# Performance work log

Measured on AMD Instinct MI355X. Metric: run time of the kernel, lower is better.

Reference implementation:

```python
import jax, jax.numpy as jnp
import numpy as np

D = 768      # d_model (BERT-base)
H = 8        # MatTransformer heads
DK = D // H  # 96
L = 4        # MatTransformer layers
FF = 1024    # MatTransformer hidden_size
NREL = 97    # num_relations
BAG = 8      # bag_len (docs per bag)
SEQ = 512    # seq_len
NB = 3       # bridge entities per doc
S = 2 + NB   # spans per doc: h, t, bridges
E = BAG * S  # total entities = 40
NEG = -1e30


def setup_inputs() -> dict:
    key = jax.random.key(0)
    ks = jax.random.split(key, 30)
    w = lambda k, shp: jax.random.normal(k, shp, jnp.float32) * 0.02
    inp = {
        "embedding": jax.random.normal(ks[0], (BAG, SEQ, D), jnp.float32),
        "spans": jnp.sort(jax.random.randint(ks[1], (BAG, S, 2), 0, SEQ, jnp.int32), axis=-1),
        # Codred pairwise-relation params (torch Linear stored as [in, out])
        "wu_w": w(ks[2], (D, D)), "wu_b": jnp.zeros((D,), jnp.float32),
        "wvv_w": w(ks[3], (D, D)), "wvv_b": jnp.zeros((D,), jnp.float32),
        "lnr_w": w(ks[4], (D, D)), "lnr_b": jnp.zeros((D,), jnp.float32),
        # MatTransformer params, stacked over layers
        "matt_wq": w(ks[5], (L, D, D)), "matt_bq": jnp.zeros((L, D), jnp.float32),
        "matt_wk": w(ks[6], (L, D, D)), "matt_bk": jnp.zeros((L, D), jnp.float32),
        "matt_wv": w(ks[7], (L, D, D)), "matt_bv": jnp.zeros((L, D), jnp.float32),
        "matt_wo": w(ks[8], (L, D, D)), "matt_bo": jnp.zeros((L, D), jnp.float32),
        "matt_w1": w(ks[9], (L, D, FF)), "matt_b1": jnp.zeros((L, FF), jnp.float32),
        "matt_w2": w(ks[10], (L, FF, D)), "matt_b2": jnp.zeros((L, D), jnp.float32),
        "matt_g1": jnp.ones((L, D), jnp.float32), "matt_be1": jnp.zeros((L, D), jnp.float32),
        "matt_g2": jnp.ones((L, D), jnp.float32), "matt_be2": jnp.zeros((L, D), jnp.float32),
        # relation predictor
        "pred_w": w(ks[11], (D, NREL)), "pred_b": jnp.zeros((NREL,), jnp.float32),
    }
    return inp


def _layernorm(x, g, b, eps=1e-5):
    m = jnp.mean(x, axis=-1, keepdims=True)
    v = jnp.var(x, axis=-1, keepdims=True)
    return (x - m) * jax.lax.rsqrt(v + eps) * g + b


def reference(embedding, spans, wu_w, wu_b, wvv_w, wvv_b, lnr_w, lnr_b,
              matt_wq, matt_bq, matt_wk, matt_bk, matt_wv, matt_bv, matt_wo, matt_bo,
              matt_w1, matt_b1, matt_w2, matt_b2, matt_g1, matt_be1, matt_g2, matt_be2,
              pred_w, pred_b):
    # --- entity span max-pool (gather + max over inclusive [start, end]) ---
    pos = jnp.arange(SEQ)
    span_mask = (pos[None, None, :] >= spans[..., 0:1]) & (pos[None, None, :] <= spans[..., 1:2])  # [BAG,S,SEQ]
    pooled = jnp.max(jnp.where(span_mask[..., None], embedding[:, None, :, :], NEG), axis=2)  # [BAG,S,D]
    htb = pooled.reshape(E, D)  # per-doc order: h, t, b1..bNB (matches htb_embs stacking)

    # --- pairwise relation matrix: relu(ln1(relu(u_i + v_j))) ---
    u = htb @ wu_w + wu_b                       # [E,D]
    v = htb @ wvv_w + wvv_b                     # [E,D]
    alpha = jax.nn.relu(u[:, None, :] + v[None, :, :])          # [E,E,D]
    rel = jax.nn.relu(alpha @ lnr_w + lnr_b)                    # [E,E,D]

    # --- MatTransformer: encoder over the E*E relation tokens (rel_mask all ones) ---
    T = E * E
    x = rel.reshape(T, D)
    scale = 1.0 / np.sqrt(DK).astype(np.float32)
    for l in range(L):
        q = (x @ matt_wq[l] + matt_bq[l]).reshape(T, H, DK)
        k = (x @ matt_wk[l] + matt_bk[l]).reshape(T, H, DK)
        vv = (x @ matt_wv[l] + matt_bv[l]).reshape(T, H, DK)
        scores = jnp.einsum('thd,shd->hts', q, k) * scale       # [H,T,T]
        attn = jax.nn.softmax(scores, axis=-1)
        o = jnp.einsum('hts,shd->thd', attn, vv).reshape(T, D)
        o = o @ matt_wo[l] + matt_bo[l]
        x = _layernorm(x + o, matt_g1[l], matt_be1[l])
        ff = jax.nn.relu(x @ matt_w1[l] + matt_b1[l]) @ matt_w2[l] + matt_b2[l]
        x = _layernorm(x + ff, matt_g2[l], matt_be2[l])
    rel_m = x.reshape(E, E, D)

    # --- gather (h, t) relation features, predict, bag max-pool over logits ---
    h_pos = jnp.arange(BAG) * S      # head entity index per doc
    t_pos = h_pos + 1                # tail entity index per doc
    ht_feat = rel_m[h_pos, t_pos]    # [BAG,D]
    ht_logits = ht_feat @ pred_w + pred_b          # [BAG,NREL]
    bag_logit = jnp.max(ht_logits, axis=0, keepdims=True)  # [1,NREL]
    return bag_logit
```

## Files before the change

### kernel.cpp

```cpp
#include <hip/hip_runtime.h>


#define D    768
#define H    8
#define DKD  96
#define LAY  4
#define FFD  1024
#define NREL 97
#define BAG  8
#define SPANS 5
#define E    40
#define TT   1600
#define SEQ  512
#define D3   2304
#define NS   3

typedef __attribute__((ext_vector_type(8))) short bf16x8;
typedef __attribute__((ext_vector_type(4))) float f32x4;
typedef unsigned short ushort_t;
typedef unsigned int uint_t;

__device__ __forceinline__ ushort_t f2b(float x) {
    uint_t u = __builtin_bit_cast(uint_t, x);
    return (ushort_t)((u + 0x7fffu + ((u >> 16) & 1u)) >> 16);
}
__device__ __forceinline__ float b2f(ushort_t v) {
    return __builtin_bit_cast(float, (uint_t)v << 16);
}

__device__ __forceinline__ void gload16(const void* g, void* l) {
    __builtin_amdgcn_global_load_lds(
        (const __attribute__((address_space(1))) unsigned int*)g,
        (__attribute__((address_space(3))) unsigned int*)l, 16, 0, 0);
}

__device__ __forceinline__ float block_sum(float v, float* red) {
#pragma unroll
    for (int o = 32; o >= 1; o >>= 1) v += __shfl_xor(v, o);
    __syncthreads();
    if ((threadIdx.x & 63) == 0) red[threadIdx.x >> 6] = v;
    __syncthreads();
    return red[0] + red[1] + red[2] + red[3];
}

__global__ __launch_bounds__(256) void span_pool_p1(const float* __restrict__ emb,
        const int* __restrict__ spans, float* __restrict__ partial) {
    const int e = blockIdx.x, pg = blockIdx.y;
    const int bag = e / SPANS;
    const int st = spans[e * 2 + 0];
    const int en = spans[e * 2 + 1];
    const int p0 = max(st, pg * 64);
    const int p1 = min(en, pg * 64 + 63);
    const int tid = threadIdx.x;
    if (tid >= 192) return;
    float4 m = make_float4(-1e30f, -1e30f, -1e30f, -1e30f);
    for (int p = p0; p <= p1; ++p) {
        const float4 v = *(const float4*)(emb + ((size_t)bag * SEQ + p) * D + tid * 4);
        m.x = fmaxf(m.x, v.x); m.y = fmaxf(m.y, v.y);
        m.z = fmaxf(m.z, v.z); m.w = fmaxf(m.w, v.w);
    }
    *(float4*)(partial + ((size_t)e * 8 + pg) * D + tid * 4) = m;
}

__global__ __launch_bounds__(256) void span_pool_p2(const float* __restrict__ partial,
        ushort_t* __restrict__ htb) {
    const int e = blockIdx.x;
    const int tid = threadIdx.x;
    if (tid >= 192) return;
    float4 m = make_float4(-1e30f, -1e30f, -1e30f, -1e30f);
#pragma unroll
    for (int pg = 0; pg < 8; ++pg) {
        const float4 v = *(const float4*)(partial + ((size_t)e * 8 + pg) * D + tid * 4);
        m.x = fmaxf(m.x, v.x); m.y = fmaxf(m.y, v.y);
        m.z = fmaxf(m.z, v.z); m.w = fmaxf(m.w, v.w);
    }
    ushort4 o;
    o.x = f2b(m.x); o.y = f2b(m.y); o.z = f2b(m.z); o.w = f2b(m.w);
    *(ushort4*)(htb + (size_t)e * D + tid * 4) = o;
}

__global__ __launch_bounds__(256) void alpha_k(const float* __restrict__ uv,
        ushort_t* __restrict__ a) {
    const int ij = blockIdx.x;
    const int i = ij / E, j = ij % E;
    const int tid = threadIdx.x;
#pragma unroll
    for (int t2 = 0; t2 < 3; ++t2) {
        const int d = tid + t2 * 256;
        a[(size_t)ij * D + d] =
            f2b(fmaxf(uv[(size_t)i * 1536 + d] + uv[(size_t)j * 1536 + 768 + d], 0.f));
    }
}

__global__ __launch_bounds__(256) void transpose_up(const float* __restrict__ lnr,
        const float* __restrict__ wu, const float* __restrict__ wvv,
        ushort_t* __restrict__ lnrT, ushort_t* __restrict__ wuvT) {
    __shared__ float t[32][33];
    const int z = blockIdx.z;
    const float* src = (z == 0) ? lnr : (z == 1) ? wu : wvv;
    ushort_t* dst = (z == 0) ? lnrT : wuvT + (size_t)(z - 1) * D * D;
    const int n0 = blockIdx.x * 32, k0 = blockIdx.y * 32;
    const int tx = threadIdx.x & 31, ty = threadIdx.x >> 5;
#pragma unroll
    for (int i = 0; i < 4; ++i)
        t[ty + i * 8][tx] = src[(size_t)(k0 + ty + i * 8) * D + n0 + tx];
    __syncthreads();
#pragma unroll
    for (int i = 0; i < 4; ++i)
        dst[(size_t)(n0 + ty + i * 8) * D + k0 + tx] = f2b(t[tx][ty + i * 8]);
}

__global__ __launch_bounds__(256) void transpose_layer(const float* __restrict__ wq,
        const float* __restrict__ wk, const float* __restrict__ wv,
        const float* __restrict__ wo, const float* __restrict__ w1,
        const float* __restrict__ w2, int l, ushort_t* __restrict__ wT4,
        ushort_t* __restrict__ w1T, ushort_t* __restrict__ w2T) {
    __shared__ float t[32][33];
    const int z = blockIdx.z;
    const float* src; ushort_t* dst; int K, N;
    if (z < 4) {
        K = D; N = D;
        src = (z == 0 ? wq : z == 1 ? wk : z == 2 ? wv : wo) + (size_t)l * D * D;
        dst = wT4 + (size_t)z * D * D;
    } else if (z == 4) {
        K = D; N = FFD; src = w1 + (size_t)l * D * FFD; dst = w1T;
    } else {
        K = FFD; N = D; src = w2 + (size_t)l * FFD * D; dst = w2T;
    }
    const int n0 = blockIdx.x * 32, k0 = blockIdx.y * 32;
    if (n0 >= N || k0 >= K) return;
    const int tx = threadIdx.x & 31, ty = threadIdx.x >> 5;
#pragma unroll
    for (int i = 0; i < 4; ++i)
        t[ty + i * 8][tx] = src[(size_t)(k0 + ty + i * 8) * N + n0 + tx];
    __syncthreads();
#pragma unroll
    for (int i = 0; i < 4; ++i)
        dst[(size_t)(n0 + ty + i * 8) * K + k0 + tx] = f2b(t[tx][ty + i * 8]);
}

__global__ __launch_bounds__(256) void concat_bias(const float* __restrict__ bq,
        const float* __restrict__ bk, const float* __restrict__ bv,
        const float* __restrict__ bu, const float* __restrict__ bvv,
        float* __restrict__ bqkv, float* __restrict__ buv) {
    const int i = blockIdx.x * 256 + threadIdx.x;
    if (i < LAY * D3) {
        const int l = i / D3, j = i % D3;
        bqkv[i] = j < D ? bq[l * D + j] : j < 2 * D ? bk[l * D + j - D] : bv[l * D + j - 2 * D];
    }
    const int k = i - LAY * D3;
    if (k >= 0 && k < 2 * D) buv[k] = k < D ? bu[k] : bvv[k - D];
}

template<int RELU, int SCALEQ>
__global__ __launch_bounds__(256) void gemm_mfma(const ushort_t* __restrict__ A,
        const ushort_t* __restrict__ Bt, const float* __restrict__ bias,
        float* __restrict__ Cf, ushort_t* __restrict__ Cb, int M, int N, int K) {
    __shared__ ushort_t As[2][128 * 32];
    __shared__ ushort_t Bs[2][64 * 32];
    const int tid = threadIdx.x;
    const int lane = tid & 63, w = tid >> 6;
    const int l15 = lane & 15, lg = lane >> 4;
    const int bm = blockIdx.y * 128, bn = blockIdx.x * 64;
    const int wm = (w >> 1) * 64, wn = (w & 1) * 32;
    const int trA0 = w * 32 + (lane >> 2);
    const int trA1 = trA0 + 16;
    const int trB  = w * 16 + (lane >> 2);
    const int sc   = (lane & 3) * 8;
    const size_t rowA0 = (size_t)min(bm + trA0, M - 1) * K;
    const size_t rowA1 = (size_t)min(bm + trA1, M - 1) * K;
    const size_t rowB  = (size_t)(bn + trB) * K;

    f32x4 acc[4][2];
#pragma unroll
    for (int mi = 0; mi < 4; ++mi)
#pragma unroll
        for (int ni = 0; ni < 2; ++ni)
            acc[mi][ni] = (f32x4){0.f, 0.f, 0.f, 0.f};

    auto STAGE = [&](int buf, int k0) {
        gload16(A + rowA0 + k0 + sc, As[buf] + w * 1024);
        gload16(A + rowA1 + k0 + sc, As[buf] + w * 1024 + 512);
        gload16(Bt + rowB + k0 + sc, Bs[buf] + w * 512);
    };

    const int ntk = K / 32;
    STAGE(0, 0);
    __syncthreads();
    for (int t = 0; t < ntk; ++t) {
        const int buf = t & 1;
        if (t + 1 < ntk) STAGE(buf ^ 1, (t + 1) * 32);
        bf16x8 af[4], bfr[2];
#pragma unroll
        for (int mi = 0; mi < 4; ++mi)
            af[mi] = *(const bf16x8*)&As[buf][(wm + mi * 16 + l15) * 32 + lg * 8];
#pragma unroll
        for (int ni = 0; ni < 2; ++ni)
            bfr[ni] = *(const bf16x8*)&Bs[buf][(wn + ni * 16 + l15) * 32 + lg * 8];
        __builtin_amdgcn_s_setprio(1);
#pragma unroll
        for (int mi = 0; mi < 4; ++mi)
#pragma unroll
            for (int ni = 0; ni < 2; ++ni)
                acc[mi][ni] = __builtin_amdgcn_mfma_f32_16x16x32_bf16(
                    af[mi], bfr[ni], acc[mi][ni], 0, 0, 0);
        __builtin_amdgcn_s_setprio(0);
        __syncthreads();
    }
#pragma unroll
    for (int mi = 0; mi < 4; ++mi)
#pragma unroll
        for (int ni = 0; ni < 2; ++ni)
#pragma unroll
            for (int r = 0; r < 4; ++r) {
                const int row = bm + wm + mi * 16 + lg * 4 + r;
                if (row >= M) continue;
                const int col = bn + wn + ni * 16 + l15;
                float v = acc[mi][ni][r] + bias[col];
                if (RELU) v = fmaxf(v, 0.f);
                if (SCALEQ) { if (col < D) v *= 0.10206207261596577f; }
                if (Cf) Cf[(size_t)row * N + col] = v;
                if (Cb) Cb[(size_t)row * N + col] = f2b(v);
            }
}

__global__ __launch_bounds__(256) void attn_part(const ushort_t* __restrict__ qkv,
        ushort_t* __restrict__ Opart, float* __restrict__ ml) {
    __shared__ ushort_t Ks[64][104];
    __shared__ ushort_t Vt[96][72];
    __shared__ ushort_t Ps[4][16][72];
    const int q0 = blockIdx.x * 64;
    const int h = blockIdx.y;
    const int cch = blockIdx.z;
    const int t_lo = (cch * (TT / 64)) / NS;
    const int t_hi = ((cch + 1) * (TT / 64)) / NS;
    const int tid = threadIdx.x;
    const int lane = tid & 63, w = tid >> 6;
    const int l15 = lane & 15, lg = lane >> 4;

    int r_[3], c_[3];
#pragma unroll
    for (int i = 0; i < 3; ++i) {
        const int ch = i * 256 + tid;
        r_[i] = ch / 12; c_[i] = (ch % 12) * 8;
    }
    bf16x8 qfrag[3];
#pragma unroll
    for (int ks = 0; ks < 3; ++ks)
        qfrag[ks] = *(const bf16x8*)(qkv + (size_t)(q0 + w * 16 + l15) * D3
                                     + h * DKD + ks * 32 + lg * 8);
    uint4 kreg[3], vreg[3];
    {
        const int s0 = t_lo * 64;
#pragma unroll
        for (int i = 0; i < 3; ++i) {
            kreg[i] = *(const uint4*)(qkv + (size_t)(s0 + r_[i]) * D3 + D + h * DKD + c_[i]);
            vreg[i] = *(const uint4*)(qkv + (size_t)(s0 + r_[i]) * D3 + 2 * D + h * DKD + c_[i]);
        }
    }
    float m_run[4], l_run[4];
    f32x4 acc_o[6];
#pragma unroll
    for (int r = 0; r < 4; ++r) { m_run[r] = -1e30f; l_run[r] = 0.f; }
#pragma unroll
    for (int nt = 0; nt < 6; ++nt) acc_o[nt] = (f32x4){0.f, 0.f, 0.f, 0.f};

    for (int t = t_lo; t < t_hi; ++t) {
        __syncthreads();
#pragma unroll
        for (int i = 0; i < 3; ++i) {
            *(uint4*)&Ks[r_[i]][c_[i]] = kreg[i];
            const ushort_t* pv = (const ushort_t*)&vreg[i];
            const int kk = r_[i] ^ (((c_[i] >> 3) & 7) << 3);
#pragma unroll
            for (int j = 0; j < 8; ++j) Vt[c_[i] + j][kk] = pv[j];
        }
        __syncthreads();
        if (t + 1 < t_hi) {
            const int s0 = (t + 1) * 64;
#pragma unroll
            for (int i = 0; i < 3; ++i) {
                kreg[i] = *(const uint4*)(qkv + (size_t)(s0 + r_[i]) * D3 + D + h * DKD + c_[i]);
                vreg[i] = *(const uint4*)(qkv + (size_t)(s0 + r_[i]) * D3 + 2 * D + h * DKD + c_[i]);
            }
        }
        f32x4 accs[4];
#pragma unroll
        for (int ni = 0; ni < 4; ++ni) accs[ni] = (f32x4){0.f, 0.f, 0.f, 0.f};
        __builtin_amdgcn_s_setprio(1);
#pragma unroll
        for (int ks = 0; ks < 3; ++ks) {
#pragma unroll
            for (int ni = 0; ni < 4; ++ni) {
                const bf16x8 bk = *(const bf16x8*)&Ks[ni * 16 + l15][ks * 32 + lg * 8];
                accs[ni] = __builtin_amdgcn_mfma_f32_16x16x32_bf16(qfrag[ks], bk, accs[ni], 0, 0, 0);
            }
        }
        __builtin_amdgcn_s_setprio(0);
        float mx[4];
#pragma unroll
        for (int r = 0; r < 4; ++r) {
            mx[r] = fmaxf(fmaxf(accs[0][r], accs[1][r]), fmaxf(accs[2][r], accs[3][r]));
#pragma unroll
            for (int o = 1; o <= 8; o <<= 1) mx[r] = fmaxf(mx[r], __shfl_xor(mx[r], o));
        }
        const bool grow = (mx[0] > m_run[0] + 8.f) || (mx[1] > m_run[1] + 8.f) ||
                          (mx[2] > m_run[2] + 8.f) || (mx[3] > m_run[3] + 8.f);
        if (__any(grow)) {
#pragma unroll
            for (int r = 0; r < 4; ++r) {
                const float mnew = fmaxf(m_run[r], mx[r]);
                const float sf = __expf(m_run[r] - mnew);
                m_run[r] = mnew;
                l_run[r] *= sf;
#pragma unroll
                for (int nt = 0; nt < 6; ++nt) acc_o[nt][r] *= sf;
            }
        }
        float ps[4][4];
#pragma unroll
        for (int r = 0; r < 4; ++r) {
            float rs = 0.f;
#pragma unroll
            for (int ni = 0; ni < 4; ++ni) {
                ps[ni][r] = __expf(accs[ni][r] - m_run[r]);
                rs += ps[ni][r];
            }
#pragma unroll
            for (int o = 1; o <= 8; o <<= 1) rs += __shfl_xor(rs, o);
            l_run[r] += rs;
        }
#pragma unroll
        for (int ni = 0; ni < 4; ++ni)
#pragma unroll
            for (int r = 0; r < 4; ++r)
                Ps[w][lg * 4 + r][ni * 16 + l15] = f2b(ps[ni][r]);
        __builtin_amdgcn_s_setprio(1);
#pragma unroll
        for (int ks = 0; ks < 2; ++ks) {
            const bf16x8 ap = *(const bf16x8*)&Ps[w][l15][ks * 32 + lg * 8];
#pragma unroll
            for (int nt = 0; nt < 6; ++nt) {
                const int dim = nt * 16 + l15;
                const int kcol = (ks * 32 + lg * 8) ^ (((dim >> 3) & 7) << 3);
                const bf16x8 bv = *(const bf16x8*)&Vt[dim][kcol];
                acc_o[nt] = __builtin_amdgcn_mfma_f32_16x16x32_bf16(ap, bv, acc_o[nt], 0, 0, 0);
            }
        }
        __builtin_amdgcn_s_setprio(0);
    }
    __syncthreads();
    ushort_t* scr = &Ks[0][0] + w * (16 * 104);
#pragma unroll
    for (int nt = 0; nt < 6; ++nt)
#pragma unroll
        for (int r = 0; r < 4; ++r)
            scr[(lg * 4 + r) * 104 + nt * 16 + l15] = f2b(acc_o[nt][r]);
    const size_t obase = (((size_t)cch * H + h) * TT + q0 + w * 16) * DKD;
#pragma unroll
    for (int ch = 0; ch < 3; ++ch) {
        const int idx = ch * 64 + lane;
        const int row = idx / 12;
        const int c16 = (idx % 12) * 8;
        const uint4 v = *(const uint4*)&scr[row * 104 + c16];
        *(uint4*)(Opart + obase + (size_t)row * DKD + c16) = v;
    }
    if (l15 == 0) {
#pragma unroll
        for (int r = 0; r < 4; ++r) {
            const int row = q0 + w * 16 + lg * 4 + r;
            float2* mlp = (float2*)ml;
            mlp[((size_t)cch * H + h) * TT + row] = make_float2(m_run[r], l_run[r]);
        }
    }
}

__global__ __launch_bounds__(256) void attn_combine(const ushort_t* __restrict__ Opart,
        const float* __restrict__ ml, ushort_t* __restrict__ O) {
    const int row = blockIdx.x;
    const int tid = threadIdx.x;
    const float2* mlp = (const float2*)ml;
#pragma unroll
    for (int kk = 0; kk < 3; ++kk) {
        const int col = tid + kk * 256;
        const int h = col / DKD, d = col % DKD;
        float m[NS], l[NS], M = -1e30f;
#pragma unroll
        for (int c = 0; c < NS; ++c) {
            const float2 v = mlp[((size_t)c * H + h) * TT + row];
            m[c] = v.x; l[c] = v.y; M = fmaxf(M, m[c]);
        }
        float L = 0.f, o = 0.f;
#pragma unroll
        for (int c = 0; c < NS; ++c) {
            const float e = __expf(m[c] - M);
            L += l[c] * e;
            o += b2f(Opart[(((size_t)c * H + h) * TT + row) * DKD + d]) * e;
        }
        O[(size_t)row * D + col] = f2b(o / L);
    }
}

__global__ __launch_bounds__(256) void add_ln(float* __restrict__ x,
        const float* __restrict__ y, const float* __restrict__ g,
        const float* __restrict__ b, ushort_t* __restrict__ xb) {
    __shared__ float red[4];
    const int row = blockIdx.x;
    const int tid = threadIdx.x;
    float vals[3];
    float s = 0.f;
#pragma unroll
    for (int i = 0; i < 3; ++i) {
        const int c = tid + i * 256;
        const float t = x[(size_t)row * D + c] + y[(size_t)row * D + c];
        vals[i] = t; s += t;
    }
    const float mean = block_sum(s, red) * (1.f / 768.f);
    float s2 = 0.f;
#pragma unroll
    for (int i = 0; i < 3; ++i) { const float dd = vals[i] - mean; s2 += dd * dd; }
    const float var = block_sum(s2, red) * (1.f / 768.f);
    const float inv = rsqrtf(var + 1e-5f);
#pragma unroll
    for (int i = 0; i < 3; ++i) {
        const int c = tid + i * 256;
        const float o = (vals[i] - mean) * inv * g[c] + b[c];
        x[(size_t)row * D + c] = o;
        xb[(size_t)row * D + c] = f2b(o);
    }
}

__global__ __launch_bounds__(256) void predict_k(const float* __restrict__ x,
        const float* __restrict__ pw, const float* __restrict__ pb,
        float* __restrict__ out) {
    __shared__ float red[4];
    const int r = blockIdx.x;
    const int tid = threadIdx.x;
    float best = -1e30f;
    for (int bag = 0; bag < BAG; ++bag) {
        const int row = (bag * SPANS) * E + (bag * SPANS + 1);
        const float* f = x + (size_t)row * D;
        float acc = 0.f;
        for (int d = tid; d < D; d += 256) acc += f[d] * pw[(size_t)d * NREL + r];
        best = fmaxf(best, block_sum(acc, red));
    }
    if (tid == 0) out[r] = best + pb[r];
}

extern "C" void kernel_launch(void* const* d_in, const int* in_sizes, int n_in,
                              void* d_out, int out_size, void* d_ws, size_t ws_size,
                              hipStream_t stream) {
    const float* emb  = (const float*)d_in[0];
    const int*  spans = (const int*)d_in[1];
    const float* wu_w = (const float*)d_in[2];  const float* wu_b = (const float*)d_in[3];
    const float* wvv_w= (const float*)d_in[4];  const float* wvv_b= (const float*)d_in[5];
    const float* lnr_w= (const float*)d_in[6];  const float* lnr_b= (const float*)d_in[7];
    const float* wq = (const float*)d_in[8];    const float* bq = (const float*)d_in[9];
    const float* wk = (const float*)d_in[10];   const float* bk = (const float*)d_in[11];
    const float* wv = (const float*)d_in[12];   const float* bv = (const float*)d_in[13];
    const float* wo = (const float*)d_in[14];   const float* bo = (const float*)d_in[15];
    const float* w1 = (const float*)d_in[16];   const float* b1 = (const float*)d_in[17];
    const float* w2 = (const float*)d_in[18];   const float* b2 = (const float*)d_in[19];
    const float* g1 = (const float*)d_in[20];   const float* be1= (const float*)d_in[21];
    const float* g2 = (const float*)d_in[22];   const float* be2= (const float*)d_in[23];
    const float* pw = (const float*)d_in[24];   const float* pb = (const float*)d_in[25];

    char* cur = (char*)d_ws;
    auto alloc = [&](size_t bytes) { char* p = cur; cur += (bytes + 255) & ~(size_t)255; return p; };
    ushort_t* htb  = (ushort_t*)alloc(E * D * 2);
    float*    uvb  = (float*)alloc((size_t)E * 1536 * 4);
    float*    part = (float*)alloc((size_t)E * 8 * D * 4);
    float*    x    = (float*)alloc((size_t)TT * D * 4);
    ushort_t* xb   = (ushort_t*)alloc((size_t)TT * D * 2);
    ushort_t* qkv  = (ushort_t*)alloc((size_t)TT * D3 * 2);
    ushort_t* ob   = (ushort_t*)alloc((size_t)TT * D * 2);
    float*    tb   = (float*)alloc((size_t)TT * D * 4);
    ushort_t* fb   = (ushort_t*)alloc((size_t)TT * FFD * 2);
    ushort_t* wT4  = (ushort_t*)alloc((size_t)4 * D * D * 2);
    ushort_t* w1T  = (ushort_t*)alloc((size_t)D * FFD * 2);
    ushort_t* w2T  = (ushort_t*)alloc((size_t)FFD * D * 2);
    float*    bqkv = (float*)alloc((size_t)LAY * D3 * 4);
    float*    buv  = (float*)alloc((size_t)2 * D * 4);
    ushort_t* Opart = (ushort_t*)tb;
    float*    ml    = part;
    ushort_t* wuvT  = wT4;
    ushort_t* lnrT  = w1T;

    const int DD = D * D;

    span_pool_p1<<<dim3(E, 8), 256, 0, stream>>>(emb, spans, part);
    span_pool_p2<<<E, 256, 0, stream>>>(part, htb);
    transpose_up<<<dim3(24, 24, 3), 256, 0, stream>>>(lnr_w, wu_w, wvv_w, lnrT, wuvT);
    concat_bias<<<(LAY * D3 + 2 * D + 255) / 256, 256, 0, stream>>>(bq, bk, bv, wu_b, wvv_b, bqkv, buv);
    gemm_mfma<0, 0><<<dim3(1536 / 64, 1), 256, 0, stream>>>(htb, wuvT, buv, uvb, nullptr, E, 1536, D);
    alpha_k<<<TT, 256, 0, stream>>>(uvb, ob);
    gemm_mfma<1, 0><<<dim3(D / 64, (TT + 127) / 128), 256, 0, stream>>>(ob, lnrT, lnr_b, x, xb, TT, D, D);

    for (int l = 0; l < LAY; ++l) {
        transpose_layer<<<dim3(32, 32, 6), 256, 0, stream>>>(wq, wk, wv, wo, w1, w2, l, wT4, w1T, w2T);
        gemm_mfma<0, 1><<<dim3(D3 / 64, (TT + 127) / 128), 256, 0, stream>>>(
            xb, wT4, bqkv + l * D3, nullptr, qkv, TT, D3, D);
        attn_part<<<dim3(TT / 64, H, NS), 256, 0, stream>>>(qkv, Opart, ml);
        attn_combine<<<TT, 256, 0, stream>>>(Opart, ml, ob);
        gemm_mfma<0, 0><<<dim3(D / 64, (TT + 127) / 128), 256, 0, stream>>>(
            ob, wT4 + 3 * DD, bo + l * D, tb, nullptr, TT, D, D);
        add_ln<<<TT, 256, 0, stream>>>(x, tb, g1 + l * D, be1 + l * D, xb);
        gemm_mfma<1, 0><<<dim3(FFD / 64, (TT + 127) / 128), 256, 0, stream>>>(
            xb, w1T, b1 + l * FFD, nullptr, fb, TT, FFD, D);
        gemm_mfma<0, 0><<<dim3(D / 64, (TT + 127) / 128), 256, 0, stream>>>(
            fb, w2T, b2 + l * D, tb, nullptr, TT, D, FFD);
        add_ln<<<TT, 256, 0, stream>>>(x, tb, g2 + l * D, be2 + l * D, xb);
    }

    predict_k<<<NREL, 256, 0, stream>>>(x, pw, pb, (float*)d_out);
    (void)in_sizes; (void)n_in; (void)out_size; (void)ws_size;
}
```

Baseline: 629.7 us.

## Split-K the N=768 GEMMs and fold partial sums into wave-per-row add+LayerNorm

```diff
diff --git a/kernel.cpp b/kernel.cpp
--- a/kernel.cpp
+++ b/kernel.cpp
@@ -152,10 +152,11 @@
     if (k >= 0 && k < 2 * D) buv[k] = k < D ? bu[k] : bvv[k - D];
 }
 
-template<int RELU, int SCALEQ>
+template<int RELU, int SCALEQ, int SPLITK>
 __global__ __launch_bounds__(256) void gemm_mfma(const ushort_t* __restrict__ A,
         const ushort_t* __restrict__ Bt, const float* __restrict__ bias,
-        float* __restrict__ Cf, ushort_t* __restrict__ Cb, int M, int N, int K) {
+        float* __restrict__ Cf, float* __restrict__ Cf1,
+        ushort_t* __restrict__ Cb, int M, int N, int K) {
     __shared__ ushort_t As[2][128 * 32];
     __shared__ ushort_t Bs[2][64 * 32];
     const int tid = threadIdx.x;
@@ -170,6 +171,8 @@
     const size_t rowA0 = (size_t)min(bm + trA0, M - 1) * K;
     const size_t rowA1 = (size_t)min(bm + trA1, M - 1) * K;
     const size_t rowB  = (size_t)(bn + trB) * K;
+    const int kbeg = SPLITK ? blockIdx.z * (K / 2) : 0;
+    const int kend = SPLITK ? kbeg + K / 2 : K;
 
     f32x4 acc[4][2];
 #pragma unroll
@@ -184,12 +187,12 @@
         gload16(Bt + rowB + k0 + sc, Bs[buf] + w * 512);
     };
 
-    const int ntk = K / 32;
-    STAGE(0, 0);
+    const int ntk = (kend - kbeg) / 32;
+    STAGE(0, kbeg);
     __syncthreads();
     for (int t = 0; t < ntk; ++t) {
         const int buf = t & 1;
-        if (t + 1 < ntk) STAGE(buf ^ 1, (t + 1) * 32);
+        if (t + 1 < ntk) STAGE(buf ^ 1, kbeg + (t + 1) * 32);
         bf16x8 af[4], bfr[2];
 #pragma unroll
         for (int mi = 0; mi < 4; ++mi)
@@ -207,6 +210,8 @@
         __builtin_amdgcn_s_setprio(0);
         __syncthreads();
     }
+    float* Cout = (SPLITK && blockIdx.z) ? Cf1 : Cf;
+    const bool addb = !(SPLITK && blockIdx.z);
 #pragma unroll
     for (int mi = 0; mi < 4; ++mi)
 #pragma unroll
@@ -216,10 +221,10 @@
                 const int row = bm + wm + mi * 16 + lg * 4 + r;
                 if (row >= M) continue;
                 const int col = bn + wn + ni * 16 + l15;
-                float v = acc[mi][ni][r] + bias[col];
+                float v = acc[mi][ni][r] + (addb ? bias[col] : 0.f);
                 if (RELU) v = fmaxf(v, 0.f);
                 if (SCALEQ) { if (col < D) v *= 0.10206207261596577f; }
-                if (Cf) Cf[(size_t)row * N + col] = v;
+                if (Cout) Cout[(size_t)row * N + col] = v;
                 if (Cb) Cb[(size_t)row * N + col] = f2b(v);
             }
 }
@@ -401,32 +406,43 @@
     }
 }
 
-__global__ __launch_bounds__(256) void add_ln(float* __restrict__ x,
-        const float* __restrict__ y, const float* __restrict__ g,
-        const float* __restrict__ b, ushort_t* __restrict__ xb) {
-    __shared__ float red[4];
-    const int row = blockIdx.x;
-    const int tid = threadIdx.x;
-    float vals[3];
-    float s = 0.f;
+__global__ __launch_bounds__(256) void add_ln3(float* __restrict__ x,
+        const float* __restrict__ y0, const float* __restrict__ y1,
+        const float* __restrict__ g, const float* __restrict__ b,
+        ushort_t* __restrict__ xb) {
+    const int lane = threadIdx.x & 63, w = threadIdx.x >> 6;
+    const int row = blockIdx.x * 4 + w;
+    const size_t base = (size_t)row * D;
+    float4 t[3];
+    float s = 0.f, s2 = 0.f;
 #pragma unroll
     for (int i = 0; i < 3; ++i) {
-        const int c = tid + i * 256;
-        const float t = x[(size_t)row * D + c] + y[(size_t)row * D + c];
-        vals[i] = t; s += t;
-    }
-    const float mean = block_sum(s, red) * (1.f / 768.f);
-    float s2 = 0.f;
-#pragma unroll
-    for (int i = 0; i < 3; ++i) { const float dd = vals[i] - mean; s2 += dd * dd; }
-    const float var = block_sum(s2, red) * (1.f / 768.f);
+        const int c = lane * 4 + i * 256;
+        const float4 xv = *(const float4*)(x + base + c);
+        const float4 a0 = *(const float4*)(y0 + base + c);
+        const float4 a1 = *(const float4*)(y1 + base + c);
+        t[i].x = xv.x + a0.x + a1.x; t[i].y = xv.y + a0.y + a1.y;
+        t[i].z = xv.z + a0.z + a1.z; t[i].w = xv.w + a0.w + a1.w;
+        s += t[i].x + t[i].y + t[i].z + t[i].w;
+        s2 += t[i].x * t[i].x + t[i].y * t[i].y + t[i].z * t[i].z + t[i].w * t[i].w;
+    }
+#pragma unroll
+    for (int o = 32; o >= 1; o >>= 1) { s += __shfl_xor(s, o); s2 += __shfl_xor(s2, o); }
+    const float mean = s * (1.f / 768.f);
+    const float var = s2 * (1.f / 768.f) - mean * mean;
     const float inv = rsqrtf(var + 1e-5f);
 #pragma unroll
     for (int i = 0; i < 3; ++i) {
-        const int c = tid + i * 256;
-        const float o = (vals[i] - mean) * inv * g[c] + b[c];
-        x[(size_t)row * D + c] = o;
-        xb[(size_t)row * D + c] = f2b(o);
+        const int c = lane * 4 + i * 256;
+        float4 o4;
+        o4.x = (t[i].x - mean) * inv * g[c + 0] + b[c + 0];
+        o4.y = (t[i].y - mean) * inv * g[c + 1] + b[c + 1];
+        o4.z = (t[i].z - mean) * inv * g[c + 2] + b[c + 2];
+        o4.w = (t[i].w - mean) * inv * g[c + 3] + b[c + 3];
+        *(float4*)(x + base + c) = o4;
+        ushort4 u;
+        u.x = f2b(o4.x); u.y = f2b(o4.y); u.z = f2b(o4.z); u.w = f2b(o4.w);
+        *(ushort4*)(xb + base + c) = u;
     }
 }
 
@@ -485,6 +501,7 @@
     float*    ml    = part;
     ushort_t* wuvT  = wT4;
     ushort_t* lnrT  = w1T;
+    float*    tb1   = (float*)qkv;
 
     const int DD = D * D;
 
@@ -492,24 +509,26 @@
     span_pool_p2<<<E, 256, 0, stream>>>(part, htb);
     transpose_up<<<dim3(24, 24, 3), 256, 0, stream>>>(lnr_w, wu_w, wvv_w, lnrT, wuvT);
     concat_bias<<<(LAY * D3 + 2 * D + 255) / 256, 256, 0, stream>>>(bq, bk, bv, wu_b, wvv_b, bqkv, buv);
-    gemm_mfma<0, 0><<<dim3(1536 / 64, 1), 256, 0, stream>>>(htb, wuvT, buv, uvb, nullptr, E, 1536, D);
+    gemm_mfma<0, 0, 0><<<dim3(1536 / 64, 1), 256, 0, stream>>>(
+        htb, wuvT, buv, uvb, nullptr, nullptr, E, 1536, D);
     alpha_k<<<TT, 256, 0, stream>>>(uvb, ob);
-    gemm_mfma<1, 0><<<dim3(D / 64, (TT + 127) / 128), 256, 0, stream>>>(ob, lnrT, lnr_b, x, xb, TT, D, D);
+    gemm_mfma<1, 0, 0><<<dim3(D / 64, (TT + 127) / 128), 256, 0, stream>>>(
+        ob, lnrT, lnr_b, x, nullptr, xb, TT, D, D);
 
     for (int l = 0; l < LAY; ++l) {
         transpose_layer<<<dim3(32, 32, 6), 256, 0, stream>>>(wq, wk, wv, wo, w1, w2, l, wT4, w1T, w2T);
-        gemm_mfma<0, 1><<<dim3(D3 / 64, (TT + 127) / 128), 256, 0, stream>>>(
-            xb, wT4, bqkv + l * D3, nullptr, qkv, TT, D3, D);
+        gemm_mfma<0, 1, 0><<<dim3(D3 / 64, (TT + 127) / 128), 256, 0, stream>>>(
+            xb, wT4, bqkv + l * D3, nullptr, nullptr, qkv, TT, D3, D);
         attn_part<<<dim3(TT / 64, H, NS), 256, 0, stream>>>(qkv, Opart, ml);
         attn_combine<<<TT, 256, 0, stream>>>(Opart, ml, ob);
-        gemm_mfma<0, 0><<<dim3(D / 64, (TT + 127) / 128), 256, 0, stream>>>(
-            ob, wT4 + 3 * DD, bo + l * D, tb, nullptr, TT, D, D);
-        add_ln<<<TT, 256, 0, stream>>>(x, tb, g1 + l * D, be1 + l * D, xb);
-        gemm_mfma<1, 0><<<dim3(FFD / 64, (TT + 127) / 128), 256, 0, stream>>>(
-            xb, w1T, b1 + l * FFD, nullptr, fb, TT, FFD, D);
-        gemm_mfma<0, 0><<<dim3(D / 64, (TT + 127) / 128), 256, 0, stream>>>(
-            fb, w2T, b2 + l * D, tb, nullptr, TT, D, FFD);
-        add_ln<<<TT, 256, 0, stream>>>(x, tb, g2 + l * D, be2 + l * D, xb);
+        gemm_mfma<0, 0, 1><<<dim3(D / 64, (TT + 127) / 128, 2), 256, 0, stream>>>(
+            ob, wT4 + 3 * DD, bo + l * D, tb, tb1, nullptr, TT, D, D);
+        add_ln3<<<TT / 4, 256, 0, stream>>>(x, tb, tb1, g1 + l * D, be1 + l * D, xb);
+        gemm_mfma<1, 0, 0><<<dim3(FFD / 64, (TT + 127) / 128), 256, 0, stream>>>(
+            xb, w1T, b1 + l * FFD, nullptr, nullptr, fb, TT, FFD, D);
+        gemm_mfma<0, 0, 1><<<dim3(D / 64, (TT + 127) / 128, 2), 256, 0, stream>>>(
+            fb, w2T, b2 + l * D, tb, tb1, nullptr, TT, D, FFD);
+        add_ln3<<<TT / 4, 256, 0, stream>>>(x, tb, tb1, g2 + l * D, be2 + l * D, xb);
     }
 
     predict_k<<<NREL, 256, 0, stream>>>(x, pw, pb, (float*)d_out);
```

New measurement: 599.9 us. 1.05x faster.
